# Kernel optimization log

Hardware: AMD Instinct MI355X
Metric: run time of the kernel (lower is better)

Reference implementation:

```python
import jax, jax.numpy as jnp
import numpy as np

N = 50000
NEG_SLOPE = 0.2  # PyG GATConv default


def _add_self_loops(edge_index, n):
    loop = jnp.arange(n, dtype=edge_index.dtype)
    src = jnp.concatenate([edge_index[0], loop])
    dst = jnp.concatenate([edge_index[1], loop])
    return src, dst


def _gat_layer(x, src, dst, W, a_src, a_dst, b, concat):
    n = x.shape[0]
    H, C = a_src.shape
    h = (x @ W).reshape(n, H, C)                      # [N,H,C]
    s_src = jnp.sum(h * a_src, axis=-1)               # [N,H] per-node src score
    s_dst = jnp.sum(h * a_dst, axis=-1)               # [N,H] per-node dst score
    e = jax.nn.leaky_relu(s_src[src] + s_dst[dst], NEG_SLOPE)  # [E,H]
    m = jax.ops.segment_max(e, dst, num_segments=n)   # segment softmax (stable)
    ex = jnp.exp(e - m[dst])
    denom = jax.ops.segment_sum(ex, dst, num_segments=n)
    alpha = ex / denom[dst]                           # [E,H]
    out = jax.ops.segment_sum(h[src] * alpha[:, :, None], dst, num_segments=n)
    out = out.reshape(n, H * C) if concat else out.mean(axis=1)
    return out + b


def setup_inputs() -> dict:
    key = jax.random.key(0)
    ks = jax.random.split(key, 10)
    in_dim, hid, heads1, out_dim, heads2 = 256, 16, 8, 64, 1
    x = jax.random.normal(ks[0], (N, in_dim), dtype=jnp.float32)
    edge_index = jax.random.randint(ks[1], (2, 800000), 0, N, dtype=jnp.int64)
    sc1 = 1.0 / np.sqrt(in_dim)
    sc2 = 1.0 / np.sqrt(hid * heads1)
    W1 = jax.random.normal(ks[2], (in_dim, heads1 * hid), dtype=jnp.float32) * sc1
    a1_src = jax.random.normal(ks[3], (heads1, hid), dtype=jnp.float32) * sc1
    a1_dst = jax.random.normal(ks[4], (heads1, hid), dtype=jnp.float32) * sc1
    b1 = jnp.zeros((heads1 * hid,), dtype=jnp.float32)
    W2 = jax.random.normal(ks[5], (heads1 * hid, heads2 * out_dim), dtype=jnp.float32) * sc2
    a2_src = jax.random.normal(ks[6], (heads2, out_dim), dtype=jnp.float32) * sc2
    a2_dst = jax.random.normal(ks[7], (heads2, out_dim), dtype=jnp.float32) * sc2
    b2 = jnp.zeros((out_dim,), dtype=jnp.float32)
    return {"x": x, "edge_index": edge_index, "W1": W1, "a1_src": a1_src,
            "a1_dst": a1_dst, "b1": b1, "W2": W2, "a2_src": a2_src,
            "a2_dst": a2_dst, "b2": b2}


def reference(x, edge_index, W1, a1_src, a1_dst, b1, W2, a2_src, a2_dst, b2):
    # eval mode: dropout layers are identity
    src, dst = _add_self_loops(edge_index, x.shape[0])
    h = _gat_layer(x, src, dst, W1, a1_src, a1_dst, b1, concat=True)
    h = jax.nn.elu(h)
    out = _gat_layer(h, src, dst, W2, a2_src, a2_dst, b2, concat=False)
    return jax.nn.log_softmax(out, axis=1)
```

## Files before the change

### kernel.cpp

```cpp
#include <hip/hip_runtime.h>
#include <hip/hip_bf16.h>

typedef __attribute__((ext_vector_type(8))) short short8;
typedef __attribute__((ext_vector_type(4))) float f32x4;

#define EDGE_CHUNK 4096

__device__ __forceinline__ float lrelu(float v) { return fmaxf(v, 0.2f * v); }

__device__ __forceinline__ short bf16_hi(float f, float* back) {
    __hip_bfloat16 h = __float2bfloat16(f);
    *back = __bfloat162float(h);
    return __builtin_bit_cast(short, h);
}
__device__ __forceinline__ short f2bf(float f) {
    return __builtin_bit_cast(short, __float2bfloat16(f));
}

__global__ void packW_all(const float* __restrict__ W1, const float* __restrict__ a1s,
                          const float* __restrict__ a1d, const float* __restrict__ W2,
                          const float* __restrict__ a2s, const float* __restrict__ a2d,
                          short* __restrict__ w1hi, short* __restrict__ w1lo,
                          short* __restrict__ w2hi, short* __restrict__ w2lo) {
    int t = blockIdx.x * blockDim.x + threadIdx.x;
    if (t < 256 * 144) {
        int j = t & 7, lane = (t >> 3) & 63, tile = t >> 9;
        int nt = tile % 9, kt = tile / 9;
        int k = kt * 32 + (lane >> 4) * 8 + j;
        int c = nt * 16 + (lane & 15);
        float w;
        if (c < 128) {
            w = W1[(size_t)k * 128 + c];
        } else {
            int hh = c - 128, h = hh & 7;
            const float* a = (hh >= 8) ? a1d : a1s;
            w = 0.f;
#pragma unroll
            for (int q = 0; q < 16; q++) w += W1[(size_t)k * 128 + h * 16 + q] * a[h * 16 + q];
        }
        float back;
        w1hi[t] = bf16_hi(w, &back);
        w1lo[t] = f2bf(w - back);
    } else {
        int u = t - 256 * 144;
        if (u >= 128 * 80) return;
        int j = u & 7, lane = (u >> 3) & 63, tile = u >> 9;
        int nt = tile % 5, kt = tile / 5;
        int k = kt * 32 + (lane >> 4) * 8 + j;
        int c = nt * 16 + (lane & 15);
        float w = 0.f;
        if (c < 64) {
            w = W2[(size_t)k * 64 + c];
        } else if (c < 66) {
            const float* a = (c == 65) ? a2d : a2s;
#pragma unroll
            for (int q = 0; q < 64; q++) w += W2[(size_t)k * 64 + q] * a[q];
        }
        float back;
        w2hi[u] = bf16_hi(w, &back);
        w2lo[u] = f2bf(w - back);
    }
}

template <int K, int NT, int MODE>
__launch_bounds__(256)
__global__ void mfma_gemm(const float* __restrict__ A, const short* __restrict__ Bhi,
                          const short* __restrict__ Blo, unsigned short* __restrict__ hb,
                          float* __restrict__ s_s, float* __restrict__ s_d, int M) {
    constexpr int KT = K / 32;
    constexpr int NH = NT - 1;
    const int wave = threadIdx.x >> 6, lane = threadIdx.x & 63;
    const int row0 = (blockIdx.x * 4 + wave) * 16;
    if (row0 >= M) return;
    const int arow = row0 + (lane & 15);
    const float* ap = A + (size_t)arow * K + (lane >> 4) * 8;

    f32x4 acc[NT];
#pragma unroll
    for (int i = 0; i < NT; i++) acc[i] = (f32x4){0.f, 0.f, 0.f, 0.f};

    for (int kt = 0; kt < KT; kt++) {
        float av[8];
        *(float4*)(av)     = *(const float4*)(ap + kt * 32);
        *(float4*)(av + 4) = *(const float4*)(ap + kt * 32 + 4);
        short8 ahi, alo;
#pragma unroll
        for (int j = 0; j < 8; j++) {
            float back;
            ahi[j] = bf16_hi(av[j], &back);
            alo[j] = f2bf(av[j] - back);
        }
        const short8* bh = (const short8*)(Bhi + ((size_t)(kt * NT) * 64 + lane) * 8);
        const short8* bl = (const short8*)(Blo + ((size_t)(kt * NT) * 64 + lane) * 8);
#pragma unroll
        for (int nt = 0; nt < NT; nt++) {
            short8 bhv = bh[nt * 64];
            short8 blv = bl[nt * 64];
            acc[nt] = __builtin_amdgcn_mfma_f32_16x16x32_bf16(ahi, bhv, acc[nt], 0, 0, 0);
            acc[nt] = __builtin_amdgcn_mfma_f32_16x16x32_bf16(ahi, blv, acc[nt], 0, 0, 0);
            acc[nt] = __builtin_amdgcn_mfma_f32_16x16x32_bf16(alo, bhv, acc[nt], 0, 0, 0);
        }
    }
    const int orow0 = row0 + (lane >> 4) * 4;
    const int col = lane & 15;
#pragma unroll
    for (int nt = 0; nt < NH; nt++)
#pragma unroll
        for (int r = 0; r < 4; r++)
            hb[(size_t)(orow0 + r) * (NH * 16) + nt * 16 + col] =
                (unsigned short)f2bf(acc[nt][r]);
#pragma unroll
    for (int r = 0; r < 4; r++) {
        int orow = orow0 + r;
        float v = acc[NH][r];
        if (MODE == 1) {
            if (col < 8) s_s[orow * 8 + col] = v;
            else         s_d[orow * 8 + (col - 8)] = v;
        } else {
            if (col == 0)      s_s[orow] = v;
            else if (col == 1) s_d[orow] = v;
        }
    }
}

__global__ void hist_kernel(const int* __restrict__ ei, int E, int n, int* __restrict__ deg) {
    int slot = blockIdx.x & 7;
    int chunk = blockIdx.x >> 3;
    int lo = (int)(((long)n * slot) >> 3);
    int hi = (int)(((long)n * (slot + 1)) >> 3);
    int ET = E + n;
    int base = chunk * EDGE_CHUNK;
    int endi = min(base + EDGE_CHUNK, ET);
    for (int i = base + threadIdx.x; i < endi; i += 256) {
        int d = (i < E) ? ei[E + i] : i - E;
        if (d >= lo && d < hi) atomicAdd(&deg[d], 1);
    }
}

__global__ void scatter_kernel(const int* __restrict__ ei, int E, int n,
                               int* __restrict__ cursor, int* __restrict__ csr_src) {
    int slot = blockIdx.x & 7;
    int chunk = blockIdx.x >> 3;
    int lo = (int)(((long)n * slot) >> 3);
    int hi = (int)(((long)n * (slot + 1)) >> 3);
    int ET = E + n;
    int base = chunk * EDGE_CHUNK;
    int endi = min(base + EDGE_CHUNK, ET);
    for (int i = base + threadIdx.x; i < endi; i += 256) {
        int s, d;
        if (i < E) { s = ei[i]; d = ei[E + i]; } else { s = d = i - E; }
        if (d >= lo && d < hi) {
            int pos = atomicAdd(&cursor[d], 1);
            csr_src[pos] = s;
        }
    }
}

__global__ void scan_block(const int* __restrict__ deg, int n, int* __restrict__ incl,
                           int* __restrict__ bsum) {
    __shared__ int wsum[16];
    int i = blockIdx.x * 1024 + threadIdx.x;
    int lane = threadIdx.x & 63, wv = threadIdx.x >> 6;
    int v = (i < n) ? deg[i] : 0;
    int s = v;
#pragma unroll
    for (int off = 1; off < 64; off <<= 1) {
        int t = __shfl_up(s, off, 64);
        if (lane >= off) s += t;
    }
    if (lane == 63) wsum[wv] = s;
    __syncthreads();
    if (wv == 0) {
        int w = (lane < 16) ? wsum[lane] : 0;
#pragma unroll
        for (int off = 1; off < 16; off <<= 1) {
            int t = __shfl_up(w, off, 64);
            if (lane >= off) w += t;
        }
        if (lane < 16) wsum[lane] = w;
    }
    __syncthreads();
    int add = wv ? wsum[wv - 1] : 0;
    if (i < n) incl[i] = s + add;
    if (threadIdx.x == 1023) bsum[blockIdx.x] = s + add;
}

__global__ void scan_tops(const int* __restrict__ bsum, int nb, int* __restrict__ boff) {
    int lane = threadIdx.x;
    int v = (lane < nb) ? bsum[lane] : 0;
    int s = v;
#pragma unroll
    for (int off = 1; off < 64; off <<= 1) {
        int t = __shfl_up(s, off, 64);
        if (lane >= off) s += t;
    }
    if (lane < nb) boff[lane] = s - v;
    if (lane == 63) boff[nb] = s;
}

__global__ void scan_final(const int* __restrict__ incl, const int* __restrict__ deg,
                           const int* __restrict__ boff, int n, int nb,
                           int* __restrict__ rowptr, int* __restrict__ cursor) {
    int i = blockIdx.x * 1024 + threadIdx.x;
    if (i < n) {
        int v = boff[i >> 10] + incl[i] - deg[i];
        rowptr[i] = v;
        cursor[i] = v;
    }
    if (i == 0) rowptr[n] = boff[nb];
}

__launch_bounds__(256)
__global__ void gather1_kernel(const int* __restrict__ rowptr, const int* __restrict__ csr_src,
                               const float* __restrict__ ssrc, const float* __restrict__ sdst,
                               const unsigned short* __restrict__ h1b,
                               const float* __restrict__ b1, float* __restrict__ out1, int n) {
    int wid = blockIdx.x * 4 + (threadIdx.x >> 6);
    if (wid >= n) return;
    int lane = threadIdx.x & 63;
    int eg = lane >> 3;
    int hs = lane & 7;
    int ha = lane >> 3;
    float sd_s = sdst[wid * 8 + hs];
    int beg = rowptr[wid], end = rowptr[wid + 1];
    float den_p = 0.f, a0 = 0.f, a1 = 0.f;

    int idx0 = beg + eg;
    int src_c = (idx0 < end) ? csr_src[idx0] : 0;
    int src_n = (idx0 + 8 < end) ? csr_src[idx0 + 8] : 0;
    float sc_c = (idx0 < end) ? ssrc[src_c * 8 + hs] : 0.f;

    for (int i = beg; i < end; i += 8) {
        int src_n2 = (i + 16 + eg < end) ? csr_src[i + 16 + eg] : 0;
        float sc_n = (i + 8 + eg < end) ? ssrc[src_n * 8 + hs] : 0.f;
        float e = (i + eg < end) ? __expf(lrelu(sc_c + sd_s)) : 0.f;
        den_p += e;
        int nn = end - i;
#define G1_BODY(k)                                                                  \
        {                                                                           \
            float eb = __shfl(e, (k) * 8 + ha, 64);                                 \
            int sb = __shfl(src_c, (k) * 8, 64);                                    \
            unsigned xw = *(const unsigned*)(h1b + (size_t)sb * 128 + 2 * lane);    \
            a0 = __builtin_fmaf(eb, __uint_as_float(xw << 16), a0);                 \
            a1 = __builtin_fmaf(eb, __uint_as_float(xw & 0xffff0000u), a1);         \
        }
        if (nn >= 8) {
#pragma unroll
            for (int k = 0; k < 8; k++) G1_BODY(k)
        } else {
            for (int k = 0; k < nn; k++) G1_BODY(k)
        }
#undef G1_BODY
        src_c = src_n; src_n = src_n2; sc_c = sc_n;
    }
    den_p += __shfl_xor(den_p, 8, 64);
    den_p += __shfl_xor(den_p, 16, 64);
    den_p += __shfl_xor(den_p, 32, 64);
    float den = __shfl(den_p, ha, 64);
    float inv = 1.f / den;
    float2 bb = *(const float2*)(b1 + 2 * lane);
    float o0 = __builtin_fmaf(a0, inv, bb.x);
    float o1 = __builtin_fmaf(a1, inv, bb.y);
    float2 o;
    o.x = o0 > 0.f ? o0 : (__expf(o0) - 1.f);
    o.y = o1 > 0.f ? o1 : (__expf(o1) - 1.f);
    *(float2*)(out1 + (size_t)wid * 128 + 2 * lane) = o;
}

__launch_bounds__(256)
__global__ void gather2_kernel(const int* __restrict__ rowptr, const int* __restrict__ csr_src,
                               const float* __restrict__ ssrc, const float* __restrict__ sdst,
                               const unsigned short* __restrict__ h2b,
                               const float* __restrict__ b2, float* __restrict__ out, int n) {
    int wid = blockIdx.x * 4 + (threadIdx.x >> 6);
    if (wid >= n) return;
    int lane = threadIdx.x & 63;
    float sd = sdst[wid];
    int beg = rowptr[wid], end = rowptr[wid + 1];
    float den_p = 0.f, acc = 0.f;

    int idx0 = beg + lane;
    int src_c = (idx0 < end) ? csr_src[idx0] : 0;
    int src_n = (idx0 + 64 < end) ? csr_src[idx0 + 64] : 0;
    float sc_c = (idx0 < end) ? ssrc[src_c] : 0.f;

    for (int i = beg; i < end; i += 64) {
        int src_n2 = (i + 128 + lane < end) ? csr_src[i + 128 + lane] : 0;
        float sc_n = (i + 64 + lane < end) ? ssrc[src_n] : 0.f;
        float e = (i + lane < end) ? __expf(lrelu(sc_c + sd)) : 0.f;
        den_p += e;
        int nn = end - i; if (nn > 64) nn = 64;
#define G2_BODY(k)                                                                  \
        {                                                                           \
            float eb = __shfl(e, (k), 64);                                          \
            int sb = __shfl(src_c, (k), 64);                                        \
            float x = __uint_as_float(((unsigned)h2b[(size_t)sb * 64 + lane]) << 16);\
            acc = __builtin_fmaf(eb, x, acc);                                       \
        }
        int k = 0;
        for (; k + 8 <= nn; k += 8) {
#pragma unroll
            for (int u = 0; u < 8; u++) G2_BODY(k + u)
        }
        for (; k < nn; k++) G2_BODY(k)
#undef G2_BODY
        src_c = src_n; src_n = src_n2; sc_c = sc_n;
    }
#pragma unroll
    for (int off = 1; off < 64; off <<= 1) den_p += __shfl_xor(den_p, off, 64);

    float o = acc / den_p + b2[lane];
    float mx = o;
#pragma unroll
    for (int off = 32; off; off >>= 1) mx = fmaxf(mx, __shfl_xor(mx, off, 64));
    float ex = __expf(o - mx);
    float sum = ex;
#pragma unroll
    for (int off = 32; off; off >>= 1) sum += __shfl_xor(sum, off, 64);
    out[(size_t)wid * 64 + lane] = o - mx - logf(sum);
}

extern "C" void kernel_launch(void* const* d_in, const int* in_sizes, int n_in,
                              void* d_out, int out_size, void* d_ws, size_t ws_size,
                              hipStream_t stream) {
    const float* x   = (const float*)d_in[0];
    const int*   ei  = (const int*)d_in[1];
    const float* W1  = (const float*)d_in[2];
    const float* a1s = (const float*)d_in[3];
    const float* a1d = (const float*)d_in[4];
    const float* b1  = (const float*)d_in[5];
    const float* W2  = (const float*)d_in[6];
    const float* a2s = (const float*)d_in[7];
    const float* a2d = (const float*)d_in[8];
    const float* b2  = (const float*)d_in[9];
    float* out = (float*)d_out;

    const int n = in_sizes[0] / 256;
    const int E = in_sizes[1] / 2;
    const int ET = E + n;
    const int NB = (n + 1023) / 1024;
    const int NCH = (ET + EDGE_CHUNK - 1) / EDGE_CHUNK;

    float* ws = (float*)d_ws;
    float* out1 = ws;
    float* s1s  = out1 + (size_t)n * 128;
    float* s1d  = s1s + (size_t)n * 8;
    float* s2s  = s1d + (size_t)n * 8;
    float* s2d  = s2s + n;
    unsigned short* h1b = (unsigned short*)(s2d + n);
    unsigned short* h2b = h1b + (size_t)n * 128;
    int*   deg     = (int*)(h2b + (size_t)n * 64);
    int*   rowptr  = deg + n;
    int*   cursor  = rowptr + n + 1;
    int*   csr_src = cursor + n;
    int*   incl    = csr_src + ET;
    int*   bsum    = incl + n;
    int*   boff    = bsum + NB;
    short* w1hi    = (short*)(boff + NB + 1);
    short* w1lo    = w1hi + 256 * 144;
    short* w2hi    = w1lo + 256 * 144;
    short* w2lo    = w2hi + 128 * 80;

    hipMemsetAsync(deg, 0, (size_t)n * 4, stream);

    const int B = 256;

    packW_all<<<(256 * 144 + 128 * 80 + B - 1) / B, B, 0, stream>>>(
        W1, a1s, a1d, W2, a2s, a2d, w1hi, w1lo, w2hi, w2lo);

    hist_kernel<<<8 * NCH, B, 0, stream>>>(ei, E, n, deg);
    scan_block<<<NB, 1024, 0, stream>>>(deg, n, incl, bsum);
    scan_tops<<<1, 64, 0, stream>>>(bsum, NB, boff);
    scan_final<<<NB, 1024, 0, stream>>>(incl, deg, boff, n, NB, rowptr, cursor);
    scatter_kernel<<<8 * NCH, B, 0, stream>>>(ei, E, n, cursor, csr_src);

    mfma_gemm<256, 9, 1><<<(n + 63) / 64, 256, 0, stream>>>(x, w1hi, w1lo, h1b, s1s, s1d, n);
    gather1_kernel<<<(n + 3) / 4, 256, 0, stream>>>(rowptr, csr_src, s1s, s1d, h1b, b1, out1, n);

    mfma_gemm<128, 5, 2><<<(n + 63) / 64, 256, 0, stream>>>(out1, w2hi, w2lo, h2b, s2s, s2d, n);
    gather2_kernel<<<(n + 3) / 4, 256, 0, stream>>>(rowptr, csr_src, s2s, s2d, h2b, b2, out, n);
}
```

Before: 303.4 us.

## Fuse preprocessing launches and replace three-pass scan with decoupled lookback

Merges weight packing with the degree histogram into one launch. It also replaces the three-kernel scan (block scan, top scan, final) with a single decoupled-lookback scan kernel. The layer-1 GEMM runs in the same launch as the CSR scatter as independent block ranges. The aim is to cut kernel launch count and inter-kernel gaps and to overlap the compute-bound GEMM with the atomic-heavy scatter. In exchange, the lookback spin-waits on flags written by other blocks, and the heterogeneous blocks may contend for resources.

```diff
diff --git a/kernel.cpp b/kernel.cpp
--- a/kernel.cpp
+++ b/kernel.cpp
@@ -17,12 +17,12 @@
     return __builtin_bit_cast(short, __float2bfloat16(f));
 }
 
-__global__ void packW_all(const float* __restrict__ W1, const float* __restrict__ a1s,
-                          const float* __restrict__ a1d, const float* __restrict__ W2,
-                          const float* __restrict__ a2s, const float* __restrict__ a2d,
-                          short* __restrict__ w1hi, short* __restrict__ w1lo,
-                          short* __restrict__ w2hi, short* __restrict__ w2lo) {
-    int t = blockIdx.x * blockDim.x + threadIdx.x;
+
+__device__ void packW_body(const float* __restrict__ W1, const float* __restrict__ a1s,
+                           const float* __restrict__ a1d, const float* __restrict__ W2,
+                           const float* __restrict__ a2s, const float* __restrict__ a2d,
+                           short* __restrict__ w1hi, short* __restrict__ w1lo,
+                           short* __restrict__ w2hi, short* __restrict__ w2lo, int t) {
     if (t < 256 * 144) {
         int j = t & 7, lane = (t >> 3) & 63, tile = t >> 9;
         int nt = tile % 9, kt = tile / 9;
@@ -62,70 +62,10 @@
     }
 }
 
-template <int K, int NT, int MODE>
-__launch_bounds__(256)
-__global__ void mfma_gemm(const float* __restrict__ A, const short* __restrict__ Bhi,
-                          const short* __restrict__ Blo, unsigned short* __restrict__ hb,
-                          float* __restrict__ s_s, float* __restrict__ s_d, int M) {
-    constexpr int KT = K / 32;
-    constexpr int NH = NT - 1;
-    const int wave = threadIdx.x >> 6, lane = threadIdx.x & 63;
-    const int row0 = (blockIdx.x * 4 + wave) * 16;
-    if (row0 >= M) return;
-    const int arow = row0 + (lane & 15);
-    const float* ap = A + (size_t)arow * K + (lane >> 4) * 8;
-
-    f32x4 acc[NT];
-#pragma unroll
-    for (int i = 0; i < NT; i++) acc[i] = (f32x4){0.f, 0.f, 0.f, 0.f};
-
-    for (int kt = 0; kt < KT; kt++) {
-        float av[8];
-        *(float4*)(av)     = *(const float4*)(ap + kt * 32);
-        *(float4*)(av + 4) = *(const float4*)(ap + kt * 32 + 4);
-        short8 ahi, alo;
-#pragma unroll
-        for (int j = 0; j < 8; j++) {
-            float back;
-            ahi[j] = bf16_hi(av[j], &back);
-            alo[j] = f2bf(av[j] - back);
-        }
-        const short8* bh = (const short8*)(Bhi + ((size_t)(kt * NT) * 64 + lane) * 8);
-        const short8* bl = (const short8*)(Blo + ((size_t)(kt * NT) * 64 + lane) * 8);
-#pragma unroll
-        for (int nt = 0; nt < NT; nt++) {
-            short8 bhv = bh[nt * 64];
-            short8 blv = bl[nt * 64];
-            acc[nt] = __builtin_amdgcn_mfma_f32_16x16x32_bf16(ahi, bhv, acc[nt], 0, 0, 0);
-            acc[nt] = __builtin_amdgcn_mfma_f32_16x16x32_bf16(ahi, blv, acc[nt], 0, 0, 0);
-            acc[nt] = __builtin_amdgcn_mfma_f32_16x16x32_bf16(alo, bhv, acc[nt], 0, 0, 0);
-        }
-    }
-    const int orow0 = row0 + (lane >> 4) * 4;
-    const int col = lane & 15;
-#pragma unroll
-    for (int nt = 0; nt < NH; nt++)
-#pragma unroll
-        for (int r = 0; r < 4; r++)
-            hb[(size_t)(orow0 + r) * (NH * 16) + nt * 16 + col] =
-                (unsigned short)f2bf(acc[nt][r]);
-#pragma unroll
-    for (int r = 0; r < 4; r++) {
-        int orow = orow0 + r;
-        float v = acc[NH][r];
-        if (MODE == 1) {
-            if (col < 8) s_s[orow * 8 + col] = v;
-            else         s_d[orow * 8 + (col - 8)] = v;
-        } else {
-            if (col == 0)      s_s[orow] = v;
-            else if (col == 1) s_d[orow] = v;
-        }
-    }
-}
-
-__global__ void hist_kernel(const int* __restrict__ ei, int E, int n, int* __restrict__ deg) {
-    int slot = blockIdx.x & 7;
-    int chunk = blockIdx.x >> 3;
+__device__ void hist_body(const int* __restrict__ ei, int E, int n, int* __restrict__ deg,
+                          int vbid) {
+    int slot = vbid & 7;
+    int chunk = vbid >> 3;
     int lo = (int)(((long)n * slot) >> 3);
     int hi = (int)(((long)n * (slot + 1)) >> 3);
     int ET = E + n;
@@ -137,10 +77,10 @@
     }
 }
 
-__global__ void scatter_kernel(const int* __restrict__ ei, int E, int n,
-                               int* __restrict__ cursor, int* __restrict__ csr_src) {
-    int slot = blockIdx.x & 7;
-    int chunk = blockIdx.x >> 3;
+__device__ void scatter_body(const int* __restrict__ ei, int E, int n,
+                             int* __restrict__ cursor, int* __restrict__ csr_src, int vbid) {
+    int slot = vbid & 7;
+    int chunk = vbid >> 3;
     int lo = (int)(((long)n * slot) >> 3);
     int hi = (int)(((long)n * (slot + 1)) >> 3);
     int ET = E + n;
@@ -156,10 +96,92 @@
     }
 }
 
-__global__ void scan_block(const int* __restrict__ deg, int n, int* __restrict__ incl,
-                           int* __restrict__ bsum) {
+template <int K, int NT, int MODE>
+__device__ void gemm_body(const float* __restrict__ A, const short* __restrict__ Bhi,
+                          const short* __restrict__ Blo, unsigned short* __restrict__ hb,
+                          float* __restrict__ s_s, float* __restrict__ s_d, int M, int vbid) {
+    constexpr int KT = K / 32;
+    constexpr int NH = NT - 1;
+    const int wave = threadIdx.x >> 6, lane = threadIdx.x & 63;
+    const int row0 = (vbid * 4 + wave) * 16;
+    if (row0 >= M) return;
+    const int arow = row0 + (lane & 15);
+    const float* ap = A + (size_t)arow * K + (lane >> 4) * 8;
+
+    f32x4 acc[NT];
+#pragma unroll
+    for (int i = 0; i < NT; i++) acc[i] = (f32x4){0.f, 0.f, 0.f, 0.f};
+
+    for (int kt = 0; kt < KT; kt++) {
+        float av[8];
+        *(float4*)(av)     = *(const float4*)(ap + kt * 32);
+        *(float4*)(av + 4) = *(const float4*)(ap + kt * 32 + 4);
+        short8 ahi, alo;
+#pragma unroll
+        for (int j = 0; j < 8; j++) {
+            float back;
+            ahi[j] = bf16_hi(av[j], &back);
+            alo[j] = f2bf(av[j] - back);
+        }
+        const short8* bh = (const short8*)(Bhi + ((size_t)(kt * NT) * 64 + lane) * 8);
+        const short8* bl = (const short8*)(Blo + ((size_t)(kt * NT) * 64 + lane) * 8);
+#pragma unroll
+        for (int nt = 0; nt < NT; nt++) {
+            short8 bhv = bh[nt * 64];
+            short8 blv = bl[nt * 64];
+            acc[nt] = __builtin_amdgcn_mfma_f32_16x16x32_bf16(ahi, bhv, acc[nt], 0, 0, 0);
+            acc[nt] = __builtin_amdgcn_mfma_f32_16x16x32_bf16(ahi, blv, acc[nt], 0, 0, 0);
+            acc[nt] = __builtin_amdgcn_mfma_f32_16x16x32_bf16(alo, bhv, acc[nt], 0, 0, 0);
+        }
+    }
+    const int orow0 = row0 + (lane >> 4) * 4;
+    const int col = lane & 15;
+#pragma unroll
+    for (int nt = 0; nt < NH; nt++)
+#pragma unroll
+        for (int r = 0; r < 4; r++)
+            hb[(size_t)(orow0 + r) * (NH * 16) + nt * 16 + col] =
+                (unsigned short)f2bf(acc[nt][r]);
+#pragma unroll
+    for (int r = 0; r < 4; r++) {
+        int orow = orow0 + r;
+        float v = acc[NH][r];
+        if (MODE == 1) {
+            if (col < 8) s_s[orow * 8 + col] = v;
+            else         s_d[orow * 8 + (col - 8)] = v;
+        } else {
+            if (col == 0)      s_s[orow] = v;
+            else if (col == 1) s_d[orow] = v;
+        }
+    }
+}
+
+
+__launch_bounds__(256)
+__global__ void fused_pack_hist(const float* __restrict__ W1, const float* __restrict__ a1s,
+                                const float* __restrict__ a1d, const float* __restrict__ W2,
+                                const float* __restrict__ a2s, const float* __restrict__ a2d,
+                                short* __restrict__ w1hi, short* __restrict__ w1lo,
+                                short* __restrict__ w2hi, short* __restrict__ w2lo,
+                                const int* __restrict__ ei, int E, int n,
+                                int* __restrict__ deg, int npack) {
+    if ((int)blockIdx.x < npack) {
+        int t = blockIdx.x * 256 + threadIdx.x;
+        packW_body(W1, a1s, a1d, W2, a2s, a2d, w1hi, w1lo, w2hi, w2lo, t);
+    } else {
+        hist_body(ei, E, n, deg, blockIdx.x - npack);
+    }
+}
+
+__launch_bounds__(1024)
+__global__ void scan_lookback(const int* __restrict__ deg, int n,
+                              int* __restrict__ rowptr, int* __restrict__ cursor,
+                              int* __restrict__ flag, int* __restrict__ aggv,
+                              int* __restrict__ inclv) {
     __shared__ int wsum[16];
-    int i = blockIdx.x * 1024 + threadIdx.x;
+    __shared__ int sprefix;
+    int b = blockIdx.x;
+    int i = b * 1024 + threadIdx.x;
     int lane = threadIdx.x & 63, wv = threadIdx.x >> 6;
     int v = (i < n) ? deg[i] : 0;
     int s = v;
@@ -181,33 +203,61 @@
     }
     __syncthreads();
     int add = wv ? wsum[wv - 1] : 0;
-    if (i < n) incl[i] = s + add;
-    if (threadIdx.x == 1023) bsum[blockIdx.x] = s + add;
-}
-
-__global__ void scan_tops(const int* __restrict__ bsum, int nb, int* __restrict__ boff) {
-    int lane = threadIdx.x;
-    int v = (lane < nb) ? bsum[lane] : 0;
-    int s = v;
-#pragma unroll
-    for (int off = 1; off < 64; off <<= 1) {
-        int t = __shfl_up(s, off, 64);
-        if (lane >= off) s += t;
-    }
-    if (lane < nb) boff[lane] = s - v;
-    if (lane == 63) boff[nb] = s;
-}
-
-__global__ void scan_final(const int* __restrict__ incl, const int* __restrict__ deg,
-                           const int* __restrict__ boff, int n, int nb,
-                           int* __restrict__ rowptr, int* __restrict__ cursor) {
-    int i = blockIdx.x * 1024 + threadIdx.x;
-    if (i < n) {
-        int v = boff[i >> 10] + incl[i] - deg[i];
-        rowptr[i] = v;
-        cursor[i] = v;
-    }
-    if (i == 0) rowptr[n] = boff[nb];
+    int incl = s + add;
+    int btot = wsum[15];
+
+    if (threadIdx.x == 0) {
+        if (b == 0) {
+            __hip_atomic_store(&inclv[0], btot, __ATOMIC_RELAXED, __HIP_MEMORY_SCOPE_AGENT);
+            __hip_atomic_store(&flag[0], 2, __ATOMIC_RELEASE, __HIP_MEMORY_SCOPE_AGENT);
+            sprefix = 0;
+        } else {
+            __hip_atomic_store(&aggv[b], btot, __ATOMIC_RELAXED, __HIP_MEMORY_SCOPE_AGENT);
+            __hip_atomic_store(&flag[b], 1, __ATOMIC_RELEASE, __HIP_MEMORY_SCOPE_AGENT);
+            int run = 0, j = b - 1;
+            while (true) {
+                int f = __hip_atomic_load(&flag[j], __ATOMIC_ACQUIRE, __HIP_MEMORY_SCOPE_AGENT);
+                if (f == 2) {
+                    run += __hip_atomic_load(&inclv[j], __ATOMIC_RELAXED, __HIP_MEMORY_SCOPE_AGENT);
+                    break;
+                }
+                if (f == 1) {
+                    run += __hip_atomic_load(&aggv[j], __ATOMIC_RELAXED, __HIP_MEMORY_SCOPE_AGENT);
+                    j--;
+                }
+            }
+            __hip_atomic_store(&inclv[b], run + btot, __ATOMIC_RELAXED, __HIP_MEMORY_SCOPE_AGENT);
+            __hip_atomic_store(&flag[b], 2, __ATOMIC_RELEASE, __HIP_MEMORY_SCOPE_AGENT);
+            sprefix = run;
+        }
+    }
+    __syncthreads();
+    int ex = sprefix + incl - v;
+    if (i < n) { rowptr[i] = ex; cursor[i] = ex; }
+    if (i == n - 1) rowptr[n] = ex + v;
+}
+
+__launch_bounds__(256)
+__global__ void fused_gemm1_scatter(const float* __restrict__ x, const short* __restrict__ w1hi,
+                                    const short* __restrict__ w1lo,
+                                    unsigned short* __restrict__ h1b, float* __restrict__ s1s,
+                                    float* __restrict__ s1d, int M,
+                                    const int* __restrict__ ei, int E, int n,
+                                    int* __restrict__ cursor, int* __restrict__ csr_src,
+                                    int ngemm) {
+    if ((int)blockIdx.x < ngemm) {
+        gemm_body<256, 9, 1>(x, w1hi, w1lo, h1b, s1s, s1d, M, blockIdx.x);
+    } else {
+        scatter_body(ei, E, n, cursor, csr_src, blockIdx.x - ngemm);
+    }
+}
+
+template <int K, int NT, int MODE>
+__launch_bounds__(256)
+__global__ void mfma_gemm(const float* __restrict__ A, const short* __restrict__ Bhi,
+                          const short* __restrict__ Blo, unsigned short* __restrict__ hb,
+                          float* __restrict__ s_s, float* __restrict__ s_d, int M) {
+    gemm_body<K, NT, MODE>(A, Bhi, Blo, hb, s_s, s_d, M, blockIdx.x);
 }
 
 __launch_bounds__(256)
@@ -340,6 +390,8 @@
     const int ET = E + n;
     const int NB = (n + 1023) / 1024;
     const int NCH = (ET + EDGE_CHUNK - 1) / EDGE_CHUNK;
+    const int NPACK = (256 * 144 + 128 * 80) / 256;
+    const int NGEMM1 = ((n + 63) / 64 + 7) & ~7;
 
     float* ws = (float*)d_ws;
     float* out1 = ws;
@@ -350,33 +402,28 @@
     unsigned short* h1b = (unsigned short*)(s2d + n);
     unsigned short* h2b = h1b + (size_t)n * 128;
     int*   deg     = (int*)(h2b + (size_t)n * 64);
-    int*   rowptr  = deg + n;
+    int*   flag    = deg + n;
+    int*   aggv    = flag + NB;
+    int*   inclv   = aggv + NB;
+    int*   rowptr  = inclv + NB;
     int*   cursor  = rowptr + n + 1;
     int*   csr_src = cursor + n;
-    int*   incl    = csr_src + ET;
-    int*   bsum    = incl + n;
-    int*   boff    = bsum + NB;
-    short* w1hi    = (short*)(boff + NB + 1);
+    short* w1hi    = (short*)(csr_src + ET);
     short* w1lo    = w1hi + 256 * 144;
     short* w2hi    = w1lo + 256 * 144;
     short* w2lo    = w2hi + 128 * 80;
 
-    hipMemsetAsync(deg, 0, (size_t)n * 4, stream);
+    hipMemsetAsync(deg, 0, (size_t)(n + NB) * 4, stream);
 
     const int B = 256;
 
-    packW_all<<<(256 * 144 + 128 * 80 + B - 1) / B, B, 0, stream>>>(
-        W1, a1s, a1d, W2, a2s, a2d, w1hi, w1lo, w2hi, w2lo);
-
-    hist_kernel<<<8 * NCH, B, 0, stream>>>(ei, E, n, deg);
-    scan_block<<<NB, 1024, 0, stream>>>(deg, n, incl, bsum);
-    scan_tops<<<1, 64, 0, stream>>>(bsum, NB, boff);
-    scan_final<<<NB, 1024, 0, stream>>>(incl, deg, boff, n, NB, rowptr, cursor);
-    scatter_kernel<<<8 * NCH, B, 0, stream>>>(ei, E, n, cursor, csr_src);
-
-    mfma_gemm<256, 9, 1><<<(n + 63) / 64, 256, 0, stream>>>(x, w1hi, w1lo, h1b, s1s, s1d, n);
+    fused_pack_hist<<<NPACK + 8 * NCH, B, 0, stream>>>(W1, a1s, a1d, W2, a2s, a2d,
+                                                       w1hi, w1lo, w2hi, w2lo,
+                                                       ei, E, n, deg, NPACK);
+    scan_lookback<<<NB, 1024, 0, stream>>>(deg, n, rowptr, cursor, flag, aggv, inclv);
+    fused_gemm1_scatter<<<NGEMM1 + 8 * NCH, B, 0, stream>>>(x, w1hi, w1lo, h1b, s1s, s1d, n,
+                                                            ei, E, n, cursor, csr_src, NGEMM1);
     gather1_kernel<<<(n + 3) / 4, 256, 0, stream>>>(rowptr, csr_src, s1s, s1d, h1b, b1, out1, n);
-
     mfma_gemm<128, 5, 2><<<(n + 63) / 64, 256, 0, stream>>>(out1, w2hi, w2lo, h2b, s2s, s2d, n);
     gather2_kernel<<<(n + 3) / 4, 256, 0, stream>>>(rowptr, csr_src, s2s, s2d, h2b, b2, out, n);
 }
```

Result: faster. 291.4 us (-3.9%).
